# Kernel tuning notes

Measured on AMD Instinct MI355X. Metric: run time of the kernel, lower is better.

## Reference

```python
import jax, jax.numpy as jnp
import numpy as np

NUM_HEADS = 16

def setup_inputs() -> dict:
    key = jax.random.key(0)
    ks = jax.random.split(key, 8)
    T, B, E = 2048, 2, 1024
    s = 1.0 / np.sqrt(E)
    return {
        "query": jax.random.normal(ks[0], (T, B, E), jnp.float32),
        "key": jax.random.normal(ks[1], (T, B, E), jnp.float32),
        "value": jax.random.normal(ks[2], (T, B, E), jnp.float32),
        "Wq": jax.random.normal(ks[3], (E, E), jnp.float32) * s,
        "bq": jnp.zeros((E,), jnp.float32),
        "Wk": jax.random.normal(ks[4], (E, E), jnp.float32) * s,
        "bk": jnp.zeros((E,), jnp.float32),
        "Wv": jax.random.normal(ks[5], (E, E), jnp.float32) * s,
        "bv": jnp.zeros((E,), jnp.float32),
        "Wo": jax.random.normal(ks[6], (E, E), jnp.float32) * s,
        "bo": jnp.zeros((E,), jnp.float32),
    }

def reference(query, key, value, Wq, bq, Wk, bk, Wv, bv, Wo, bo):
    T, B, E = query.shape
    S = key.shape[0]
    H = NUM_HEADS
    hd = E // H
    scaling = float(hd) ** -0.5
    # linear projections (torch Linear: x @ W.T + b)
    q = (query @ Wq.T + bq).reshape(T, B, H, hd)
    k = (key @ Wk.T + bk).reshape(S, B, H, hd)
    v = (value @ Wv.T + bv).reshape(S, B, H, hd)
    # scores: (B, H, T, S)
    scores = jnp.einsum('tbhd,sbhd->bhts', q, k) * scaling
    attn = jax.nn.softmax(scores, axis=-1)  # dropout p=0
    # weighted sum: (T, B, H, hd) -> (T, B, E)
    out = jnp.einsum('bhts,sbhd->tbhd', attn, v).reshape(T, B, E)
    out = out @ Wo.T + bo
    # averaged attention weights over heads: (B, T, S)
    avg_w = attn.mean(axis=1)
    return (out, avg_w)
```

## Files before the change

kernel.cpp:

```cpp
#include <hip/hip_runtime.h>
#include <hip/hip_bf16.h>
#include <stdint.h>

#define HN 16
#define TT 2048
#define BBATCH 2
#define EE 1024
#define HD 64
#define MM 4096

#define SCALEQ 0.18033688011112042f

typedef __attribute__((ext_vector_type(8))) __bf16 bfrag;
typedef __attribute__((ext_vector_type(4))) float f32x4;
typedef __attribute__((ext_vector_type(4))) short s16x4;

__device__ __forceinline__ void gll16(const void* g, void* lds) {
  __builtin_amdgcn_global_load_lds(
      (const __attribute__((address_space(1))) void*)g,
      (__attribute__((address_space(3))) void*)lds, 16, 0, 0);
}

__device__ __forceinline__ f32x4 mfma_bf16(bfrag a, bfrag b, f32x4 c) {
  return __builtin_amdgcn_mfma_f32_16x16x32_bf16(a, b, c, 0, 0, 0);
}

__device__ __forceinline__ const bfrag* fragp(const __bf16* base, int row, int e) {
  return (const bfrag*)(base + row * 64 + ((((e >> 3) ^ row) & 7) << 3));
}
__device__ __forceinline__ void stage8(const __bf16* grow0, int gstride,
                                       __bf16* tile, int r0, int lane) {
  const int rr = lane >> 3;
  const int cl = (lane & 7) ^ rr;
  gll16(grow0 + (size_t)(r0 + rr) * gstride + cl * 8, tile + r0 * 64);
}

__device__ __forceinline__ void barrier_fence() {
  __builtin_amdgcn_s_barrier();
  __builtin_amdgcn_sched_barrier(0);
}

struct CvtArgs {
  const float* src[7];
  __bf16* dst[7];
  int n4[7];
};

__global__ __launch_bounds__(256) void cvt_all(CvtArgs a) {
  const int z = blockIdx.z;
  const int i = blockIdx.x * 256 + threadIdx.x;
  if (i < a.n4[z]) {
    float4 v = ((const float4*)a.src[z])[i];
    struct alignas(8) B4 { __bf16 a0, a1, a2, a3; };
    B4 o = {(__bf16)v.x, (__bf16)v.y, (__bf16)v.z, (__bf16)v.w};
    ((B4*)a.dst[z])[i] = o;
  }
}

template <int MT>
__device__ __forceinline__ void gemm2(const __bf16* __restrict__ X,
                                      const __bf16* __restrict__ W,
                                      const float* __restrict__ bias,
                                      void* __restrict__ out, int mode,
                                      float scale, int m0, int n0,
                                      __bf16* As0, __bf16* As1,
                                      __bf16* Bs0, __bf16* Bs1) {
  const int tid = threadIdx.x, lane = tid & 63, w = tid >> 6;
  const int wm = w >> 1, wn = w & 1;
  const int quad = lane >> 4, l16 = lane & 15;
  constexpr int FM = MT / 32;
  constexpr int NLD = FM + 4;

  auto stageAB = [&](int buf, int k0) {
    __bf16* A = buf ? As1 : As0;
    __bf16* B = buf ? Bs1 : Bs0;
    #pragma unroll
    for (int c = 0; c < FM; ++c)
      stage8(X + (size_t)m0 * EE + k0, EE, A, w * (MT / 4) + c * 8, lane);
    #pragma unroll
    for (int c = 0; c < 4; ++c)
      stage8(W + (size_t)n0 * EE + k0, EE, B, w * 32 + c * 8, lane);
  };

  stageAB(0, 0);

  f32x4 acc[FM][4] = {};

  for (int it = 0; it < EE / 64; ++it) {
    const int cur = it & 1;
    barrier_fence();
    if (it + 1 < EE / 64) {
      stageAB(1 - cur, (it + 1) * 64);
      asm volatile("s_waitcnt vmcnt(%0)" :: "n"(NLD) : "memory");
    } else {
      asm volatile("s_waitcnt vmcnt(0)" ::: "memory");
    }
    barrier_fence();

    const __bf16* A = cur ? As1 : As0;
    const __bf16* B = cur ? Bs1 : Bs0;
    #pragma unroll
    for (int ks = 0; ks < 2; ++ks) {
      bfrag a[FM], b[4];
      #pragma unroll
      for (int f = 0; f < FM; ++f)
        a[f] = *fragp(A, wm * (MT / 2) + f * 16 + l16, ks * 32 + quad * 8);
      #pragma unroll
      for (int f = 0; f < 4; ++f)
        b[f] = *fragp(B, wn * 64 + f * 16 + l16, ks * 32 + quad * 8);
      #pragma unroll
      for (int fm = 0; fm < FM; ++fm)
        #pragma unroll
        for (int fn = 0; fn < 4; ++fn)
          acc[fm][fn] = mfma_bf16(a[fm], b[fn], acc[fm][fn]);
    }
  }

  float bv[4];
  #pragma unroll
  for (int fn = 0; fn < 4; ++fn) bv[fn] = bias[n0 + wn * 64 + fn * 16 + l16];

  #pragma unroll
  for (int fm = 0; fm < FM; ++fm) {
    #pragma unroll
    for (int r = 0; r < 4; ++r) {
      const int gm = m0 + wm * (MT / 2) + fm * 16 + quad * 4 + r;
      #pragma unroll
      for (int fn = 0; fn < 4; ++fn) {
        const int gn = n0 + wn * 64 + fn * 16 + l16;
        const float v = (acc[fm][fn][r] + bv[fn]) * scale;
        if (mode == 0) {
          const int t = gm >> 1, bb = gm & 1, h = gn >> 6, d = gn & 63;
          ((__bf16*)out)[(((size_t)(bb * HN + h)) * TT + t) * HD + d] = (__bf16)v;
        } else if (mode == 2) {
          const int s = gm >> 1, bb = gm & 1, h = gn >> 6, d = gn & 63;
          ((__bf16*)out)[(((size_t)(bb * HN + h)) * HD + d) * TT + s] = (__bf16)v;
        } else {
          ((float*)out)[(size_t)gm * EE + gn] = v;
        }
      }
    }
  }
}

__global__ __launch_bounds__(256, 2) void gemm_qkv(
    const __bf16* __restrict__ xq, const __bf16* __restrict__ xk,
    const __bf16* __restrict__ xv, const __bf16* __restrict__ wq,
    const __bf16* __restrict__ wk, const __bf16* __restrict__ wv,
    const float* __restrict__ bq, const float* __restrict__ bk,
    const float* __restrict__ bv, __bf16* __restrict__ qo,
    __bf16* __restrict__ ko, __bf16* __restrict__ vo) {
  __shared__ __bf16 As[2][128 * 64];
  __shared__ __bf16 Bs[2][128 * 64];
  const int bx = blockIdx.x;
  const int m = bx & 31, n = (bx >> 5) & 7, z = bx >> 8;
  const __bf16 *X, *W;
  const float* bias;
  __bf16* out;
  int mode;
  float scale;
  if (z == 0)      { X = xq; W = wq; bias = bq; out = qo; mode = 0; scale = SCALEQ; }
  else if (z == 1) { X = xk; W = wk; bias = bk; out = ko; mode = 0; scale = 1.0f; }
  else             { X = xv; W = wv; bias = bv; out = vo; mode = 2; scale = 1.0f; }
  gemm2<128>(X, W, bias, out, mode, scale, m * 128, n * 128,
             As[0], As[1], Bs[0], Bs[1]);
}

__global__ __launch_bounds__(256, 2) void attn_fwd(const __bf16* __restrict__ qb,
                                                   const __bf16* __restrict__ kb,
                                                   const __bf16* __restrict__ vtb,
                                                   __bf16* __restrict__ ob,
                                                   float* __restrict__ linv_ws) {
  union Sh {
    __bf16 kv[2][2][2][64 * 64];
    float om[2][64 * 64];
  };
  __shared__ Sh sm;
  __shared__ float Lsum[2][128];
  __shared__ float LinvS[128];

  const int tid = threadIdx.x, lane = tid & 63, w = tid >> 6;
  const int p = w >> 1, tw = w & 1;
  const int quad = lane >> 4, l16 = lane & 15;

  const int bx = blockIdx.x;
  const int xcd = bx & 7, slot = bx >> 3;
  const int bhi = xcd * 4 + (slot >> 4);
  const int t0 = (slot & 15) * 128;
  const int b = bhi >> 4, h = bhi & 15;
  const size_t bh = (size_t)(b * HN + h);

  const __bf16* qbase = qb + (bh * TT + t0) * HD;
  const __bf16* kbase = kb + bh * TT * HD;
  const __bf16* vbase = vtb + bh * HD * TT;
  const int sBase = p * 1024;

  #pragma unroll
  for (int c = 0; c < 4; ++c) {
    stage8(kbase + (size_t)sBase * HD, HD, sm.kv[p][0][0], tw * 32 + c * 8, lane);
    stage8(vbase + sBase, TT, sm.kv[p][1][0], tw * 32 + c * 8, lane);
  }

  bfrag qf[4][2];
  #pragma unroll
  for (int fn = 0; fn < 4; ++fn)
    #pragma unroll
    for (int ks = 0; ks < 2; ++ks)
      qf[fn][ks] = *(const bfrag*)(qbase +
          (size_t)(tw * 64 + fn * 16 + l16) * HD + ks * 32 + quad * 8);

  bfrag ones;
  {
    union { short s[8]; bfrag v; } u;
    #pragma unroll
    for (int i = 0; i < 8; ++i) u.s[i] = 0x3F80;
    ones = u.v;
  }

  f32x4 oacc[4][4] = {};
  f32x4 lacc[4] = {};

  for (int it = 0; it < 16; ++it) {
    const int cur = it & 1;
    barrier_fence();
    if (it + 1 < 16) {
      const int s1 = sBase + (it + 1) * 64;
      #pragma unroll
      for (int c = 0; c < 4; ++c) {
        stage8(kbase + (size_t)s1 * HD, HD, sm.kv[p][0][1 - cur], tw * 32 + c * 8, lane);
        stage8(vbase + s1, TT, sm.kv[p][1][1 - cur], tw * 32 + c * 8, lane);
      }
      asm volatile("s_waitcnt vmcnt(8)" ::: "memory");
    } else {
      asm volatile("s_waitcnt vmcnt(0)" ::: "memory");
    }
    barrier_fence();

    f32x4 sacc[4][4] = {};
    #pragma unroll
    for (int ks = 0; ks < 2; ++ks) {
      bfrag kf[4];
      #pragma unroll
      for (int fm = 0; fm < 4; ++fm)
        kf[fm] = *fragp(sm.kv[p][0][cur], fm * 16 + l16, ks * 32 + quad * 8);
      #pragma unroll
      for (int fm = 0; fm < 4; ++fm)
        #pragma unroll
        for (int fn = 0; fn < 4; ++fn)
          sacc[fm][fn] = mfma_bf16(kf[fm], qf[fn][ks], sacc[fm][fn]);
    }

    union PB { __bf16 hh[8]; bfrag v; } pb[2][4];
    #pragma unroll
    for (int fm = 0; fm < 4; ++fm)
      #pragma unroll
      for (int fn = 0; fn < 4; ++fn) {
        const float p0 = __builtin_amdgcn_exp2f(sacc[fm][fn][0]);
        const float p1 = __builtin_amdgcn_exp2f(sacc[fm][fn][1]);
        const float p2 = __builtin_amdgcn_exp2f(sacc[fm][fn][2]);
        const float p3 = __builtin_amdgcn_exp2f(sacc[fm][fn][3]);
        const int hb = (fm & 1) * 4;
        pb[fm >> 1][fn].hh[hb + 0] = (__bf16)p0;
        pb[fm >> 1][fn].hh[hb + 1] = (__bf16)p1;
        pb[fm >> 1][fn].hh[hb + 2] = (__bf16)p2;
        pb[fm >> 1][fn].hh[hb + 3] = (__bf16)p3;
      }

    #pragma unroll
    for (int ks = 0; ks < 2; ++ks) {
      bfrag vf[4];
      #pragma unroll
      for (int fm = 0; fm < 4; ++fm) {
        const __bf16* base = sm.kv[p][1][cur] + (fm * 16 + l16) * 64;
        const int sw = l16 & 7, qh = quad >> 1, qo = (quad & 1) * 4;
        union VF { s16x4 q[2]; bfrag v; } u;
        u.q[0] = *(const s16x4*)(base + (((ks * 4 + qh) ^ sw) << 3) + qo);
        u.q[1] = *(const s16x4*)(base + (((ks * 4 + 2 + qh) ^ sw) << 3) + qo);
        vf[fm] = u.v;
      }
      #pragma unroll
      for (int fn = 0; fn < 4; ++fn)
        lacc[fn] = mfma_bf16(ones, pb[ks][fn].v, lacc[fn]);
      #pragma unroll
      for (int fm = 0; fm < 4; ++fm)
        #pragma unroll
        for (int fn = 0; fn < 4; ++fn)
          oacc[fm][fn] = mfma_bf16(vf[fm], pb[ks][fn].v, oacc[fm][fn]);
    }
  }

  if (quad == 0)
    #pragma unroll
    for (int fn = 0; fn < 4; ++fn)
      Lsum[p][tw * 64 + fn * 16 + l16] = lacc[fn][0];

  __syncthreads();

  if (p == 1) {
    #pragma unroll
    for (int fm = 0; fm < 4; ++fm)
      #pragma unroll
      for (int fn = 0; fn < 4; ++fn)
        #pragma unroll
        for (int r = 0; r < 4; ++r)
          sm.om[tw][(fm * 16 + quad * 4 + r) * 64 + fn * 16 + l16] = oacc[fm][fn][r];
  }
  if (tid < 128) {
    const float linv = 1.0f / (Lsum[0][tid] + Lsum[1][tid]);
    LinvS[tid] = linv;
    linv_ws[bh * TT + t0 + tid] = linv;
  }
  __syncthreads();

  if (p == 0) {
    float li[4];
    #pragma unroll
    for (int fn = 0; fn < 4; ++fn) li[fn] = LinvS[tw * 64 + fn * 16 + l16];
    #pragma unroll
    for (int fm = 0; fm < 4; ++fm)
      #pragma unroll
      for (int fn = 0; fn < 4; ++fn) {
        const int t = t0 + tw * 64 + fn * 16 + l16;
        struct alignas(8) B4 { __bf16 a0, a1, a2, a3; };
        B4 o;
        __bf16* op = &o.a0;
        #pragma unroll
        for (int r = 0; r < 4; ++r) {
          const float v = (oacc[fm][fn][r] +
              sm.om[tw][(fm * 16 + quad * 4 + r) * 64 + fn * 16 + l16]) * li[fn];
          op[r] = (__bf16)v;
        }
        *(B4*)(ob + ((size_t)t * BBATCH + b) * EE + h * HD + fm * 16 + quad * 4) = o;
      }
  }
}

__device__ __forceinline__ void avg_body(const __bf16* __restrict__ qb,
                                         const __bf16* __restrict__ kb,
                                         const float* __restrict__ linv_ws,
                                         float* __restrict__ avg_out, int bx,
                                         __bf16* Qs0, __bf16* Qs1,
                                         __bf16* Ks0, __bf16* Ks1) {
  const int tid = threadIdx.x, lane = tid & 63, w = tid >> 6;
  const int wm = w >> 1, wn = w & 1;
  const int quad = lane >> 4, l16 = lane & 15;

  const int xcd = bx & 7, slot = bx >> 3;
  const int bti = xcd * 4 + (slot >> 4);
  const int s0 = (slot & 15) * 128;
  const int b = bti >> 4, t0 = (bti & 15) * 128;

  const __bf16* qt = qb + (((size_t)b * HN) * TT + t0) * HD;
  const __bf16* kt = kb + (((size_t)b * HN) * TT + s0) * HD;
  const float* lrow0 = linv_ws + ((size_t)b * HN) * TT + t0 + wm * 64;

  #pragma unroll
  for (int c = 0; c < 4; ++c) {
    stage8(qt, HD, Qs0, w * 32 + c * 8, lane);
    stage8(kt, HD, Ks0, w * 32 + c * 8, lane);
  }

  f32x4 aacc[4][4] = {};

  for (int h = 0; h < HN; ++h) {
    const int cur = h & 1;
    barrier_fence();
    if (h + 1 < HN) {
      const __bf16* qn = qt + (size_t)(h + 1) * TT * HD;
      const __bf16* kn = kt + (size_t)(h + 1) * TT * HD;
      __bf16* Qn = cur ? Qs0 : Qs1;
      __bf16* Kn = cur ? Ks0 : Ks1;
      #pragma unroll
      for (int c = 0; c < 4; ++c) {
        stage8(qn, HD, Qn, w * 32 + c * 8, lane);
        stage8(kn, HD, Kn, w * 32 + c * 8, lane);
      }
      asm volatile("s_waitcnt vmcnt(8)" ::: "memory");
    } else {
      asm volatile("s_waitcnt vmcnt(0)" ::: "memory");
    }
    barrier_fence();

    const __bf16* Qc = cur ? Qs1 : Qs0;
    const __bf16* Kc = cur ? Ks1 : Ks0;
    f32x4 sacc[4][4] = {};
    #pragma unroll
    for (int ks = 0; ks < 2; ++ks) {
      bfrag qf4[4], kf4[4];
      #pragma unroll
      for (int f = 0; f < 4; ++f)
        qf4[f] = *fragp(Qc, wm * 64 + f * 16 + l16, ks * 32 + quad * 8);
      #pragma unroll
      for (int f = 0; f < 4; ++f)
        kf4[f] = *fragp(Kc, wn * 64 + f * 16 + l16, ks * 32 + quad * 8);
      #pragma unroll
      for (int fm = 0; fm < 4; ++fm)
        #pragma unroll
        for (int fn = 0; fn < 4; ++fn)
          sacc[fm][fn] = mfma_bf16(qf4[fm], kf4[fn], sacc[fm][fn]);
    }

    const float* lr = lrow0 + (size_t)h * TT;
    f32x4 lvv[4];
    #pragma unroll
    for (int fm = 0; fm < 4; ++fm)
      lvv[fm] = *(const f32x4*)(lr + fm * 16 + quad * 4);

    #pragma unroll
    for (int fm = 0; fm < 4; ++fm)
      #pragma unroll
      for (int fn = 0; fn < 4; ++fn)
        #pragma unroll
        for (int r = 0; r < 4; ++r)
          aacc[fm][fn][r] += __builtin_amdgcn_exp2f(sacc[fm][fn][r]) * lvv[fm][r];
  }

  const float invh = 1.0f / (float)HN;
  #pragma unroll
  for (int fm = 0; fm < 4; ++fm)
    #pragma unroll
    for (int r = 0; r < 4; ++r) {
      const int t = t0 + wm * 64 + fm * 16 + quad * 4 + r;
      #pragma unroll
      for (int fn = 0; fn < 4; ++fn) {
        const int s = s0 + wn * 64 + fn * 16 + l16;
        avg_out[((size_t)b * TT + t) * TT + s] = aacc[fm][fn][r] * invh;
      }
    }
}

struct TailAvg { __bf16 Qs[2][128 * 64]; __bf16 Ks[2][128 * 64]; };
struct TailGo  { __bf16 As[2][64 * 64];  __bf16 Bs[2][128 * 64]; };
union TailSh { TailAvg a; TailGo g; };

__global__ __launch_bounds__(256, 2) void tail_fused(
    const __bf16* __restrict__ qb, const __bf16* __restrict__ kb,
    const float* __restrict__ linv_ws, float* __restrict__ avg_out,
    const __bf16* __restrict__ ob, const __bf16* __restrict__ wo,
    const float* __restrict__ bo, float* __restrict__ out) {
  __shared__ TailSh sh;
  const int bx = blockIdx.x;
  if (bx < 512) {
    avg_body(qb, kb, linv_ws, avg_out, bx,
             sh.a.Qs[0], sh.a.Qs[1], sh.a.Ks[0], sh.a.Ks[1]);
  } else {
    const int b2 = bx - 512;
    const int m = b2 & 63, n = b2 >> 6;
    gemm2<64>(ob, wo, bo, out, 3, 1.0f, m * 64, n * 128,
              sh.g.As[0], sh.g.As[1], sh.g.Bs[0], sh.g.Bs[1]);
  }
}

extern "C" void kernel_launch(void* const* d_in, const int* in_sizes, int n_in,
                              void* d_out, int out_size, void* d_ws, size_t ws_size,
                              hipStream_t stream) {
  (void)in_sizes; (void)n_in; (void)out_size; (void)ws_size;
  const float* query = (const float*)d_in[0];
  const float* key   = (const float*)d_in[1];
  const float* value = (const float*)d_in[2];
  const float* Wq = (const float*)d_in[3];
  const float* bq = (const float*)d_in[4];
  const float* Wk = (const float*)d_in[5];
  const float* bk = (const float*)d_in[6];
  const float* Wv = (const float*)d_in[7];
  const float* bv = (const float*)d_in[8];
  const float* Wo = (const float*)d_in[9];
  const float* bo = (const float*)d_in[10];

  char* ws = (char*)d_ws;
  size_t off = 0;
  auto wsalloc = [&](size_t bytes) -> void* {
    void* p = ws + off;
    off += (bytes + 255) & ~(size_t)255;
    return p;
  };
  const size_t XE = (size_t)MM * EE;
  const size_t WE = (size_t)EE * EE;
  __bf16* xq   = (__bf16*)wsalloc(XE * 2);
  __bf16* xk   = (__bf16*)wsalloc(XE * 2);
  __bf16* xv   = (__bf16*)wsalloc(XE * 2);
  __bf16* wqb  = (__bf16*)wsalloc(WE * 2);
  __bf16* wkb  = (__bf16*)wsalloc(WE * 2);
  __bf16* wvb  = (__bf16*)wsalloc(WE * 2);
  __bf16* wob  = (__bf16*)wsalloc(WE * 2);
  __bf16* qbuf = (__bf16*)wsalloc(XE * 2);
  __bf16* kbuf = (__bf16*)wsalloc(XE * 2);
  __bf16* vtbuf= (__bf16*)wsalloc(XE * 2);
  __bf16* obuf = (__bf16*)wsalloc(XE * 2);
  float* linv  = (float*)wsalloc((size_t)BBATCH * HN * TT * 4);

  CvtArgs ca;
  ca.src[0] = query; ca.dst[0] = xq;  ca.n4[0] = (int)(XE / 4);
  ca.src[1] = key;   ca.dst[1] = xk;  ca.n4[1] = (int)(XE / 4);
  ca.src[2] = value; ca.dst[2] = xv;  ca.n4[2] = (int)(XE / 4);
  ca.src[3] = Wq;    ca.dst[3] = wqb; ca.n4[3] = (int)(WE / 4);
  ca.src[4] = Wk;    ca.dst[4] = wkb; ca.n4[4] = (int)(WE / 4);
  ca.src[5] = Wv;    ca.dst[5] = wvb; ca.n4[5] = (int)(WE / 4);
  ca.src[6] = Wo;    ca.dst[6] = wob; ca.n4[6] = (int)(WE / 4);
  cvt_all<<<dim3(4096, 1, 7), 256, 0, stream>>>(ca);

  gemm_qkv<<<dim3(768), 256, 0, stream>>>(xq, xk, xv, wqb, wkb, wvb,
                                          bq, bk, bv, qbuf, kbuf, vtbuf);

  attn_fwd<<<dim3(512), 256, 0, stream>>>(qbuf, kbuf, vtbuf, obuf, linv);

  float* avg_out = (float*)d_out + (size_t)TT * BBATCH * EE;
  tail_fused<<<dim3(1024), 256, 0, stream>>>(qbuf, kbuf, linv, avg_out,
                                             obuf, wob, bo, (float*)d_out);
}
```

Baseline: 240.5 us.

## Fuse kernels into two persistent launches joined by grid barriers

Folds the fp32-to-bf16 conversion into the QKV GEMM kernel, and the attention kernel into the tail kernel. Each pair is separated by a software grid barrier built on an atomic counter, which cuts four launches to two and removes the inter-kernel gaps. The QKV GEMM drops double buffering for a single LDS buffer at higher occupancy. The shared GEMM helper replaces its explicit vmcnt pipelining with plain __syncthreads. The grid barriers assume every block is resident at once and can deadlock otherwise. The extra synchronisation and the loss of load/compute overlap may cost more than the launches saved.

Result: slower. 483.3 us (+100.9%).

```diff
diff --git a/kernel.cpp b/kernel.cpp
--- a/kernel.cpp
+++ b/kernel.cpp
@@ -15,6 +15,8 @@
 typedef __attribute__((ext_vector_type(4))) float f32x4;
 typedef __attribute__((ext_vector_type(4))) short s16x4;
 
+struct alignas(8) B4 { __bf16 a0, a1, a2, a3; };
+
 __device__ __forceinline__ void gll16(const void* g, void* lds) {
   __builtin_amdgcn_global_load_lds(
       (const __attribute__((address_space(1))) void*)g,
@@ -40,21 +42,19 @@
   __builtin_amdgcn_sched_barrier(0);
 }
 
-struct CvtArgs {
-  const float* src[7];
-  __bf16* dst[7];
-  int n4[7];
-};
-
-__global__ __launch_bounds__(256) void cvt_all(CvtArgs a) {
-  const int z = blockIdx.z;
-  const int i = blockIdx.x * 256 + threadIdx.x;
-  if (i < a.n4[z]) {
-    float4 v = ((const float4*)a.src[z])[i];
-    struct alignas(8) B4 { __bf16 a0, a1, a2, a3; };
-    B4 o = {(__bf16)v.x, (__bf16)v.y, (__bf16)v.z, (__bf16)v.w};
-    ((B4*)a.dst[z])[i] = o;
-  }
+__device__ __forceinline__ void grid_barrier(unsigned int* ctr, unsigned int nb) {
+  __syncthreads();
+  if (threadIdx.x == 0) {
+    __threadfence();
+    unsigned int old = __hip_atomic_fetch_add(ctr, 1u, __ATOMIC_RELEASE,
+                                              __HIP_MEMORY_SCOPE_AGENT);
+    unsigned int target = old - (old % nb) + nb;
+    while (__hip_atomic_load(ctr, __ATOMIC_ACQUIRE,
+                             __HIP_MEMORY_SCOPE_AGENT) < target)
+      __builtin_amdgcn_s_sleep(2);
+    __threadfence();
+  }
+  __syncthreads();
 }
 
 template <int MT>
@@ -69,7 +69,6 @@
   const int wm = w >> 1, wn = w & 1;
   const int quad = lane >> 4, l16 = lane & 15;
   constexpr int FM = MT / 32;
-  constexpr int NLD = FM + 4;
 
   auto stageAB = [&](int buf, int k0) {
     __bf16* A = buf ? As1 : As0;
@@ -88,14 +87,8 @@
 
   for (int it = 0; it < EE / 64; ++it) {
     const int cur = it & 1;
-    barrier_fence();
-    if (it + 1 < EE / 64) {
-      stageAB(1 - cur, (it + 1) * 64);
-      asm volatile("s_waitcnt vmcnt(%0)" :: "n"(NLD) : "memory");
-    } else {
-      asm volatile("s_waitcnt vmcnt(0)" ::: "memory");
-    }
-    barrier_fence();
+    __syncthreads();
+    if (it + 1 < EE / 64) stageAB(1 - cur, (it + 1) * 64);
 
     const __bf16* A = cur ? As1 : As0;
     const __bf16* B = cur ? Bs1 : Bs0;
@@ -143,15 +136,39 @@
   }
 }
 
-__global__ __launch_bounds__(256, 2) void gemm_qkv(
-    const __bf16* __restrict__ xq, const __bf16* __restrict__ xk,
-    const __bf16* __restrict__ xv, const __bf16* __restrict__ wq,
-    const __bf16* __restrict__ wk, const __bf16* __restrict__ wv,
-    const float* __restrict__ bq, const float* __restrict__ bk,
-    const float* __restrict__ bv, __bf16* __restrict__ qo,
-    __bf16* __restrict__ ko, __bf16* __restrict__ vo) {
-  __shared__ __bf16 As[2][128 * 64];
-  __shared__ __bf16 Bs[2][128 * 64];
+struct Fused1 {
+  const float* src[7];
+  __bf16* dst[7];
+  const float* bias[3];
+  __bf16* outp[3];
+  unsigned int* ctr;
+};
+
+__global__ __launch_bounds__(256, 4) void cvt_gemm_qkv(Fused1 a) {
+  __shared__ __bf16 As[128 * 64];
+  __shared__ __bf16 Bs[128 * 64];
+
+  {
+    const int gtid = blockIdx.x * 256 + threadIdx.x;
+    const int gstr = 768 * 256;
+    for (int z = 0; z < 7; ++z) {
+      const int n4 = (z < 3) ? (1 << 20) : (1 << 18);
+      const float4* s = (const float4*)a.src[z];
+      B4* d = (B4*)a.dst[z];
+      for (int i = gtid; i < n4; i += gstr) {
+        float4 v = s[i];
+        B4 o = {(__bf16)v.x, (__bf16)v.y, (__bf16)v.z, (__bf16)v.w};
+        d[i] = o;
+      }
+    }
+  }
+
+  grid_barrier(a.ctr, 768);
+
+  const int tid = threadIdx.x, lane = tid & 63, w = tid >> 6;
+  const int wm = w >> 1, wn = w & 1;
+  const int quad = lane >> 4, l16 = lane & 15;
+
   const int bx = blockIdx.x;
   const int m = bx & 31, n = (bx >> 5) & 7, z = bx >> 8;
   const __bf16 *X, *W;
@@ -159,31 +176,80 @@
   __bf16* out;
   int mode;
   float scale;
-  if (z == 0)      { X = xq; W = wq; bias = bq; out = qo; mode = 0; scale = SCALEQ; }
-  else if (z == 1) { X = xk; W = wk; bias = bk; out = ko; mode = 0; scale = 1.0f; }
-  else             { X = xv; W = wv; bias = bv; out = vo; mode = 2; scale = 1.0f; }
-  gemm2<128>(X, W, bias, out, mode, scale, m * 128, n * 128,
-             As[0], As[1], Bs[0], Bs[1]);
-}
-
-__global__ __launch_bounds__(256, 2) void attn_fwd(const __bf16* __restrict__ qb,
-                                                   const __bf16* __restrict__ kb,
-                                                   const __bf16* __restrict__ vtb,
-                                                   __bf16* __restrict__ ob,
-                                                   float* __restrict__ linv_ws) {
-  union Sh {
-    __bf16 kv[2][2][2][64 * 64];
-    float om[2][64 * 64];
-  };
-  __shared__ Sh sm;
-  __shared__ float Lsum[2][128];
-  __shared__ float LinvS[128];
-
+  if (z == 0)      { X = a.dst[0]; W = a.dst[3]; bias = a.bias[0]; out = a.outp[0]; mode = 0; scale = SCALEQ; }
+  else if (z == 1) { X = a.dst[1]; W = a.dst[4]; bias = a.bias[1]; out = a.outp[1]; mode = 0; scale = 1.0f; }
+  else             { X = a.dst[2]; W = a.dst[5]; bias = a.bias[2]; out = a.outp[2]; mode = 2; scale = 1.0f; }
+  const int m0 = m * 128, n0 = n * 128;
+
+  f32x4 acc[4][4] = {};
+
+  for (int it = 0; it < 16; ++it) {
+    const int k0 = it * 64;
+    #pragma unroll
+    for (int c = 0; c < 4; ++c)
+      stage8(X + (size_t)m0 * EE + k0, EE, As, w * 32 + c * 8, lane);
+    #pragma unroll
+    for (int c = 0; c < 4; ++c)
+      stage8(W + (size_t)n0 * EE + k0, EE, Bs, w * 32 + c * 8, lane);
+    __syncthreads();
+    #pragma unroll
+    for (int ks = 0; ks < 2; ++ks) {
+      bfrag af[4], bf[4];
+      #pragma unroll
+      for (int f = 0; f < 4; ++f)
+        af[f] = *fragp(As, wm * 64 + f * 16 + l16, ks * 32 + quad * 8);
+      #pragma unroll
+      for (int f = 0; f < 4; ++f)
+        bf[f] = *fragp(Bs, wn * 64 + f * 16 + l16, ks * 32 + quad * 8);
+      #pragma unroll
+      for (int fm = 0; fm < 4; ++fm)
+        #pragma unroll
+        for (int fn = 0; fn < 4; ++fn)
+          acc[fm][fn] = mfma_bf16(af[fm], bf[fn], acc[fm][fn]);
+    }
+    __syncthreads();
+  }
+
+  float bvv[4];
+  #pragma unroll
+  for (int fn = 0; fn < 4; ++fn) bvv[fn] = bias[n0 + wn * 64 + fn * 16 + l16];
+
+  #pragma unroll
+  for (int fm = 0; fm < 4; ++fm) {
+    #pragma unroll
+    for (int r = 0; r < 4; ++r) {
+      const int gm = m0 + wm * 64 + fm * 16 + quad * 4 + r;
+      #pragma unroll
+      for (int fn = 0; fn < 4; ++fn) {
+        const int gn = n0 + wn * 64 + fn * 16 + l16;
+        const float v = (acc[fm][fn][r] + bvv[fn]) * scale;
+        if (mode == 0) {
+          const int t = gm >> 1, bb = gm & 1, h = gn >> 6, d = gn & 63;
+          out[(((size_t)(bb * HN + h)) * TT + t) * HD + d] = (__bf16)v;
+        } else {
+          const int s = gm >> 1, bb = gm & 1, h = gn >> 6, d = gn & 63;
+          out[(((size_t)(bb * HN + h)) * HD + d) * TT + s] = (__bf16)v;
+        }
+      }
+    }
+  }
+}
+
+struct AttnSh {
+  union { __bf16 kv[2][2][2][64 * 64]; float om[2][64 * 64]; } u;
+  float Lsum[2][128];
+  float LinvS[128];
+};
+
+__device__ void attn_body(const __bf16* __restrict__ qb,
+                          const __bf16* __restrict__ kb,
+                          const __bf16* __restrict__ vtb,
+                          __bf16* __restrict__ ob,
+                          float* __restrict__ linv_ws, int bx, AttnSh& sa) {
   const int tid = threadIdx.x, lane = tid & 63, w = tid >> 6;
   const int p = w >> 1, tw = w & 1;
   const int quad = lane >> 4, l16 = lane & 15;
 
-  const int bx = blockIdx.x;
   const int xcd = bx & 7, slot = bx >> 3;
   const int bhi = xcd * 4 + (slot >> 4);
   const int t0 = (slot & 15) * 128;
@@ -197,8 +263,8 @@
 
   #pragma unroll
   for (int c = 0; c < 4; ++c) {
-    stage8(kbase + (size_t)sBase * HD, HD, sm.kv[p][0][0], tw * 32 + c * 8, lane);
-    stage8(vbase + sBase, TT, sm.kv[p][1][0], tw * 32 + c * 8, lane);
+    stage8(kbase + (size_t)sBase * HD, HD, sa.u.kv[p][0][0], tw * 32 + c * 8, lane);
+    stage8(vbase + sBase, TT, sa.u.kv[p][1][0], tw * 32 + c * 8, lane);
   }
 
   bfrag qf[4][2];
@@ -227,8 +293,8 @@
       const int s1 = sBase + (it + 1) * 64;
       #pragma unroll
       for (int c = 0; c < 4; ++c) {
-        stage8(kbase + (size_t)s1 * HD, HD, sm.kv[p][0][1 - cur], tw * 32 + c * 8, lane);
-        stage8(vbase + s1, TT, sm.kv[p][1][1 - cur], tw * 32 + c * 8, lane);
+        stage8(kbase + (size_t)s1 * HD, HD, sa.u.kv[p][0][1 - cur], tw * 32 + c * 8, lane);
+        stage8(vbase + s1, TT, sa.u.kv[p][1][1 - cur], tw * 32 + c * 8, lane);
       }
       asm volatile("s_waitcnt vmcnt(8)" ::: "memory");
     } else {
@@ -242,7 +308,7 @@
       bfrag kf[4];
       #pragma unroll
       for (int fm = 0; fm < 4; ++fm)
-        kf[fm] = *fragp(sm.kv[p][0][cur], fm * 16 + l16, ks * 32 + quad * 8);
+        kf[fm] = *fragp(sa.u.kv[p][0][cur], fm * 16 + l16, ks * 32 + quad * 8);
       #pragma unroll
       for (int fm = 0; fm < 4; ++fm)
         #pragma unroll
@@ -271,7 +337,7 @@
       bfrag vf[4];
       #pragma unroll
       for (int fm = 0; fm < 4; ++fm) {
-        const __bf16* base = sm.kv[p][1][cur] + (fm * 16 + l16) * 64;
+        const __bf16* base = sa.u.kv[p][1][cur] + (fm * 16 + l16) * 64;
         const int sw = l16 & 7, qh = quad >> 1, qo = (quad & 1) * 4;
         union VF { s16x4 q[2]; bfrag v; } u;
         u.q[0] = *(const s16x4*)(base + (((ks * 4 + qh) ^ sw) << 3) + qo);
@@ -292,7 +358,7 @@
   if (quad == 0)
     #pragma unroll
     for (int fn = 0; fn < 4; ++fn)
-      Lsum[p][tw * 64 + fn * 16 + l16] = lacc[fn][0];
+      sa.Lsum[p][tw * 64 + fn * 16 + l16] = lacc[fn][0];
 
   __syncthreads();
 
@@ -303,11 +369,11 @@
       for (int fn = 0; fn < 4; ++fn)
         #pragma unroll
         for (int r = 0; r < 4; ++r)
-          sm.om[tw][(fm * 16 + quad * 4 + r) * 64 + fn * 16 + l16] = oacc[fm][fn][r];
+          sa.u.om[tw][(fm * 16 + quad * 4 + r) * 64 + fn * 16 + l16] = oacc[fm][fn][r];
   }
   if (tid < 128) {
-    const float linv = 1.0f / (Lsum[0][tid] + Lsum[1][tid]);
-    LinvS[tid] = linv;
+    const float linv = 1.0f / (sa.Lsum[0][tid] + sa.Lsum[1][tid]);
+    sa.LinvS[tid] = linv;
     linv_ws[bh * TT + t0 + tid] = linv;
   }
   __syncthreads();
@@ -315,19 +381,18 @@
   if (p == 0) {
     float li[4];
     #pragma unroll
-    for (int fn = 0; fn < 4; ++fn) li[fn] = LinvS[tw * 64 + fn * 16 + l16];
+    for (int fn = 0; fn < 4; ++fn) li[fn] = sa.LinvS[tw * 64 + fn * 16 + l16];
     #pragma unroll
     for (int fm = 0; fm < 4; ++fm)
       #pragma unroll
       for (int fn = 0; fn < 4; ++fn) {
         const int t = t0 + tw * 64 + fn * 16 + l16;
-        struct alignas(8) B4 { __bf16 a0, a1, a2, a3; };
         B4 o;
         __bf16* op = &o.a0;
         #pragma unroll
         for (int r = 0; r < 4; ++r) {
           const float v = (oacc[fm][fn][r] +
-              sm.om[tw][(fm * 16 + quad * 4 + r) * 64 + fn * 16 + l16]) * li[fn];
+              sa.u.om[tw][(fm * 16 + quad * 4 + r) * 64 + fn * 16 + l16]) * li[fn];
           op[r] = (__bf16)v;
         }
         *(B4*)(ob + ((size_t)t * BBATCH + b) * EE + h * HD + fm * 16 + quad * 4) = o;
@@ -335,12 +400,12 @@
   }
 }
 
-__device__ __forceinline__ void avg_body(const __bf16* __restrict__ qb,
-                                         const __bf16* __restrict__ kb,
-                                         const float* __restrict__ linv_ws,
-                                         float* __restrict__ avg_out, int bx,
-                                         __bf16* Qs0, __bf16* Qs1,
-                                         __bf16* Ks0, __bf16* Ks1) {
+__device__ void avg_body(const __bf16* __restrict__ qb,
+                         const __bf16* __restrict__ kb,
+                         const float* __restrict__ linv_ws,
+                         float* __restrict__ avg_out, int bx,
+                         __bf16* Qs0, __bf16* Qs1,
+                         __bf16* Ks0, __bf16* Ks1) {
   const int tid = threadIdx.x, lane = tid & 63, w = tid >> 6;
   const int wm = w >> 1, wn = w & 1;
   const int quad = lane >> 4, l16 = lane & 15;
@@ -431,22 +496,33 @@
 
 struct TailAvg { __bf16 Qs[2][128 * 64]; __bf16 Ks[2][128 * 64]; };
 struct TailGo  { __bf16 As[2][64 * 64];  __bf16 Bs[2][128 * 64]; };
-union TailSh { TailAvg a; TailGo g; };
-
-__global__ __launch_bounds__(256, 2) void tail_fused(
+union Sh2 { AttnSh at; TailAvg a; TailGo g; };
+
+__global__ __launch_bounds__(256, 2) void attn_tail(
     const __bf16* __restrict__ qb, const __bf16* __restrict__ kb,
-    const float* __restrict__ linv_ws, float* __restrict__ avg_out,
-    const __bf16* __restrict__ ob, const __bf16* __restrict__ wo,
-    const float* __restrict__ bo, float* __restrict__ out) {
-  __shared__ TailSh sh;
+    const __bf16* __restrict__ vtb, __bf16* __restrict__ ob,
+    float* __restrict__ linv_ws, float* __restrict__ avg_out,
+    const __bf16* __restrict__ wo, const float* __restrict__ bo,
+    float* __restrict__ out, unsigned int* ctr) {
+  __shared__ Sh2 sh;
   const int bx = blockIdx.x;
-  if (bx < 512) {
+
+  attn_body(qb, kb, vtb, ob, linv_ws, bx, sh.at);
+
+  grid_barrier(ctr, 512);
+
+  const int gm_m = bx & 63, gm_n = bx >> 6;
+  if ((bx >> 8) & 1) {
+    gemm2<64>(ob, wo, bo, out, 3, 1.0f, gm_m * 64, gm_n * 128,
+              sh.g.As[0], sh.g.As[1], sh.g.Bs[0], sh.g.Bs[1]);
+    __syncthreads();
     avg_body(qb, kb, linv_ws, avg_out, bx,
              sh.a.Qs[0], sh.a.Qs[1], sh.a.Ks[0], sh.a.Ks[1]);
   } else {
-    const int b2 = bx - 512;
-    const int m = b2 & 63, n = b2 >> 6;
-    gemm2<64>(ob, wo, bo, out, 3, 1.0f, m * 64, n * 128,
+    avg_body(qb, kb, linv_ws, avg_out, bx,
+             sh.a.Qs[0], sh.a.Qs[1], sh.a.Ks[0], sh.a.Ks[1]);
+    __syncthreads();
+    gemm2<64>(ob, wo, bo, out, 3, 1.0f, gm_m * 64, gm_n * 128,
               sh.g.As[0], sh.g.As[1], sh.g.Bs[0], sh.g.Bs[1]);
   }
 }
@@ -488,23 +564,23 @@
   __bf16* vtbuf= (__bf16*)wsalloc(XE * 2);
   __bf16* obuf = (__bf16*)wsalloc(XE * 2);
   float* linv  = (float*)wsalloc((size_t)BBATCH * HN * TT * 4);
-
-  CvtArgs ca;
-  ca.src[0] = query; ca.dst[0] = xq;  ca.n4[0] = (int)(XE / 4);
-  ca.src[1] = key;   ca.dst[1] = xk;  ca.n4[1] = (int)(XE / 4);
-  ca.src[2] = value; ca.dst[2] = xv;  ca.n4[2] = (int)(XE / 4);
-  ca.src[3] = Wq;    ca.dst[3] = wqb; ca.n4[3] = (int)(WE / 4);
-  ca.src[4] = Wk;    ca.dst[4] = wkb; ca.n4[4] = (int)(WE / 4);
-  ca.src[5] = Wv;    ca.dst[5] = wvb; ca.n4[5] = (int)(WE / 4);
-  ca.src[6] = Wo;    ca.dst[6] = wob; ca.n4[6] = (int)(WE / 4);
-  cvt_all<<<dim3(4096, 1, 7), 256, 0, stream>>>(ca);
-
-  gemm_qkv<<<dim3(768), 256, 0, stream>>>(xq, xk, xv, wqb, wkb, wvb,
-                                          bq, bk, bv, qbuf, kbuf, vtbuf);
-
-  attn_fwd<<<dim3(512), 256, 0, stream>>>(qbuf, kbuf, vtbuf, obuf, linv);
+  unsigned int* ctrs = (unsigned int*)wsalloc(512);
+
+  hipMemsetAsync(ctrs, 0, 512, stream);
+
+  Fused1 f1;
+  f1.src[0] = query; f1.src[1] = key; f1.src[2] = value;
+  f1.src[3] = Wq;    f1.src[4] = Wk;  f1.src[5] = Wv;  f1.src[6] = Wo;
+  f1.dst[0] = xq;    f1.dst[1] = xk;  f1.dst[2] = xv;
+  f1.dst[3] = wqb;   f1.dst[4] = wkb; f1.dst[5] = wvb; f1.dst[6] = wob;
+  f1.bias[0] = bq;   f1.bias[1] = bk; f1.bias[2] = bv;
+  f1.outp[0] = qbuf; f1.outp[1] = kbuf; f1.outp[2] = vtbuf;
+  f1.ctr = ctrs;
+
+  cvt_gemm_qkv<<<dim3(768), 256, 0, stream>>>(f1);
 
   float* avg_out = (float*)d_out + (size_t)TT * BBATCH * EE;
-  tail_fused<<<dim3(1024), 256, 0, stream>>>(qbuf, kbuf, linv, avg_out,
-                                             obuf, wob, bo, (float*)d_out);
-}
+  attn_tail<<<dim3(512), 256, 0, stream>>>(qbuf, kbuf, vtbuf, obuf, linv,
+                                           avg_out, wob, bo, (float*)d_out,
+                                           ctrs + 64);
+}
```

## Fuse fp32-to-bf16 conversion into GEMM tile loads and drop separate convert kernel

Applied to the files above, without the earlier changes.

Removes the standalone cvt_all kernel that converted inputs and weights to bf16. The QKV GEMM and the output-projection GEMM now read fp32 directly from global memory into registers, convert to bf16, and write swizzled tiles to LDS, using a register-prefetch double-buffer pipeline in place of async global_load_lds. This saves one kernel launch and a full read+write pass over about 60 MB of inputs. In exchange the GEMMs read twice as many bytes per tile, hold more registers, and do the conversion on the critical path, which could lower occupancy or MFMA utilisation.

After: 267.8 us. 1.11x slower.

```diff
diff --git a/kernel.cpp b/kernel.cpp
--- a/kernel.cpp
+++ b/kernel.cpp
@@ -15,6 +15,9 @@
 typedef __attribute__((ext_vector_type(4))) float f32x4;
 typedef __attribute__((ext_vector_type(4))) short s16x4;
 
+struct alignas(8) B4 { __bf16 a0, a1, a2, a3; };
+struct alignas(16) B8 { __bf16 h[8]; };
+
 __device__ __forceinline__ void gll16(const void* g, void* lds) {
   __builtin_amdgcn_global_load_lds(
       (const __attribute__((address_space(1))) void*)g,
@@ -40,130 +43,223 @@
   __builtin_amdgcn_sched_barrier(0);
 }
 
-struct CvtArgs {
-  const float* src[7];
-  __bf16* dst[7];
-  int n4[7];
-};
-
-__global__ __launch_bounds__(256) void cvt_all(CvtArgs a) {
-  const int z = blockIdx.z;
-  const int i = blockIdx.x * 256 + threadIdx.x;
-  if (i < a.n4[z]) {
-    float4 v = ((const float4*)a.src[z])[i];
-    struct alignas(8) B4 { __bf16 a0, a1, a2, a3; };
-    B4 o = {(__bf16)v.x, (__bf16)v.y, (__bf16)v.z, (__bf16)v.w};
-    ((B4*)a.dst[z])[i] = o;
-  }
-}
-
-template <int MT>
-__device__ __forceinline__ void gemm2(const __bf16* __restrict__ X,
-                                      const __bf16* __restrict__ W,
-                                      const float* __restrict__ bias,
-                                      void* __restrict__ out, int mode,
-                                      float scale, int m0, int n0,
-                                      __bf16* As0, __bf16* As1,
-                                      __bf16* Bs0, __bf16* Bs1) {
-  const int tid = threadIdx.x, lane = tid & 63, w = tid >> 6;
-  const int wm = w >> 1, wn = w & 1;
-  const int quad = lane >> 4, l16 = lane & 15;
-  constexpr int FM = MT / 32;
-  constexpr int NLD = FM + 4;
-
-  auto stageAB = [&](int buf, int k0) {
-    __bf16* A = buf ? As1 : As0;
-    __bf16* B = buf ? Bs1 : Bs0;
-    #pragma unroll
-    for (int c = 0; c < FM; ++c)
-      stage8(X + (size_t)m0 * EE + k0, EE, A, w * (MT / 4) + c * 8, lane);
-    #pragma unroll
-    for (int c = 0; c < 4; ++c)
-      stage8(W + (size_t)n0 * EE + k0, EE, B, w * 32 + c * 8, lane);
-  };
-
-  stageAB(0, 0);
-
-  f32x4 acc[FM][4] = {};
-
-  for (int it = 0; it < EE / 64; ++it) {
-    const int cur = it & 1;
-    barrier_fence();
-    if (it + 1 < EE / 64) {
-      stageAB(1 - cur, (it + 1) * 64);
-      asm volatile("s_waitcnt vmcnt(%0)" :: "n"(NLD) : "memory");
-    } else {
-      asm volatile("s_waitcnt vmcnt(0)" ::: "memory");
-    }
-    barrier_fence();
-
-    const __bf16* A = cur ? As1 : As0;
-    const __bf16* B = cur ? Bs1 : Bs0;
-    #pragma unroll
-    for (int ks = 0; ks < 2; ++ks) {
-      bfrag a[FM], b[4];
-      #pragma unroll
-      for (int f = 0; f < FM; ++f)
-        a[f] = *fragp(A, wm * (MT / 2) + f * 16 + l16, ks * 32 + quad * 8);
-      #pragma unroll
-      for (int f = 0; f < 4; ++f)
-        b[f] = *fragp(B, wn * 64 + f * 16 + l16, ks * 32 + quad * 8);
-      #pragma unroll
-      for (int fm = 0; fm < FM; ++fm)
-        #pragma unroll
-        for (int fn = 0; fn < 4; ++fn)
-          acc[fm][fn] = mfma_bf16(a[fm], b[fn], acc[fm][fn]);
-    }
-  }
-
-  float bv[4];
-  #pragma unroll
-  for (int fn = 0; fn < 4; ++fn) bv[fn] = bias[n0 + wn * 64 + fn * 16 + l16];
-
-  #pragma unroll
-  for (int fm = 0; fm < FM; ++fm) {
-    #pragma unroll
-    for (int r = 0; r < 4; ++r) {
-      const int gm = m0 + wm * (MT / 2) + fm * 16 + quad * 4 + r;
-      #pragma unroll
-      for (int fn = 0; fn < 4; ++fn) {
-        const int gn = n0 + wn * 64 + fn * 16 + l16;
-        const float v = (acc[fm][fn][r] + bv[fn]) * scale;
-        if (mode == 0) {
-          const int t = gm >> 1, bb = gm & 1, h = gn >> 6, d = gn & 63;
-          ((__bf16*)out)[(((size_t)(bb * HN + h)) * TT + t) * HD + d] = (__bf16)v;
-        } else if (mode == 2) {
-          const int s = gm >> 1, bb = gm & 1, h = gn >> 6, d = gn & 63;
-          ((__bf16*)out)[(((size_t)(bb * HN + h)) * HD + d) * TT + s] = (__bf16)v;
-        } else {
-          ((float*)out)[(size_t)gm * EE + gn] = v;
-        }
-      }
-    }
-  }
+__device__ __forceinline__ void lbar() {
+  __builtin_amdgcn_sched_barrier(0);
+  asm volatile("s_waitcnt lgkmcnt(0)" ::: "memory");
+  __builtin_amdgcn_s_barrier();
+  __builtin_amdgcn_sched_barrier(0);
 }
 
 __global__ __launch_bounds__(256, 2) void gemm_qkv(
-    const __bf16* __restrict__ xq, const __bf16* __restrict__ xk,
-    const __bf16* __restrict__ xv, const __bf16* __restrict__ wq,
-    const __bf16* __restrict__ wk, const __bf16* __restrict__ wv,
+    const float* __restrict__ xq, const float* __restrict__ xk,
+    const float* __restrict__ xv, const float* __restrict__ wq,
+    const float* __restrict__ wk, const float* __restrict__ wv,
     const float* __restrict__ bq, const float* __restrict__ bk,
     const float* __restrict__ bv, __bf16* __restrict__ qo,
     __bf16* __restrict__ ko, __bf16* __restrict__ vo) {
   __shared__ __bf16 As[2][128 * 64];
   __shared__ __bf16 Bs[2][128 * 64];
+  const int tid = threadIdx.x, lane = tid & 63, w = tid >> 6;
+  const int wm = w >> 1, wn = w & 1;
+  const int quad = lane >> 4, l16 = lane & 15;
+
   const int bx = blockIdx.x;
   const int m = bx & 31, n = (bx >> 5) & 7, z = bx >> 8;
-  const __bf16 *X, *W;
-  const float* bias;
+  const float *X, *W, *bias;
   __bf16* out;
   int mode;
   float scale;
   if (z == 0)      { X = xq; W = wq; bias = bq; out = qo; mode = 0; scale = SCALEQ; }
   else if (z == 1) { X = xk; W = wk; bias = bk; out = ko; mode = 0; scale = 1.0f; }
   else             { X = xv; W = wv; bias = bv; out = vo; mode = 2; scale = 1.0f; }
-  gemm2<128>(X, W, bias, out, mode, scale, m * 128, n * 128,
-             As[0], As[1], Bs[0], Bs[1]);
+  const int m0 = m * 128, n0 = n * 128;
+  const float* Xg = X + (size_t)m0 * EE;
+  const float* Wg = W + (size_t)n0 * EE;
+
+  const int rA = tid >> 3;
+  const int cc = tid & 7;
+
+  float4 vA[8], vB[8];
+
+  auto loadT = [&](const float* src, int k0, float4* dst) {
+    #pragma unroll
+    for (int i = 0; i < 4; ++i) {
+      const float* p = src + (size_t)(rA + 32 * i) * EE + k0 + cc * 8;
+      dst[2 * i]     = *(const float4*)p;
+      dst[2 * i + 1] = *(const float4*)(p + 4);
+    }
+  };
+  auto writeT = [&](__bf16* tile, const float4* v) {
+    #pragma unroll
+    for (int i = 0; i < 4; ++i) {
+      const int r = rA + 32 * i;
+      B8 o;
+      o.h[0] = (__bf16)v[2 * i].x;     o.h[1] = (__bf16)v[2 * i].y;
+      o.h[2] = (__bf16)v[2 * i].z;     o.h[3] = (__bf16)v[2 * i].w;
+      o.h[4] = (__bf16)v[2 * i + 1].x; o.h[5] = (__bf16)v[2 * i + 1].y;
+      o.h[6] = (__bf16)v[2 * i + 1].z; o.h[7] = (__bf16)v[2 * i + 1].w;
+      *(B8*)(tile + r * 64 + (((cc ^ r) & 7) << 3)) = o;
+    }
+  };
+
+  loadT(Xg, 0, vA);  loadT(Wg, 0, vB);
+  writeT(As[0], vA); writeT(Bs[0], vB);
+  loadT(Xg, 64, vA); loadT(Wg, 64, vB);
+
+  f32x4 acc[4][4] = {};
+
+  for (int it = 0; it < 16; ++it) {
+    const int cur = it & 1;
+    lbar();
+
+    const __bf16* A = As[cur];
+    const __bf16* B = Bs[cur];
+    #pragma unroll
+    for (int ks = 0; ks < 2; ++ks) {
+      bfrag af[4], bf[4];
+      #pragma unroll
+      for (int f = 0; f < 4; ++f)
+        af[f] = *fragp(A, wm * 64 + f * 16 + l16, ks * 32 + quad * 8);
+      #pragma unroll
+      for (int f = 0; f < 4; ++f)
+        bf[f] = *fragp(B, wn * 64 + f * 16 + l16, ks * 32 + quad * 8);
+      #pragma unroll
+      for (int fm = 0; fm < 4; ++fm)
+        #pragma unroll
+        for (int fn = 0; fn < 4; ++fn)
+          acc[fm][fn] = mfma_bf16(af[fm], bf[fn], acc[fm][fn]);
+    }
+
+    if (it + 1 < 16) {
+      writeT(As[1 - cur], vA);
+      writeT(Bs[1 - cur], vB);
+    }
+    if (it + 2 < 16) {
+      loadT(Xg, (it + 2) * 64, vA);
+      loadT(Wg, (it + 2) * 64, vB);
+    }
+  }
+
+  float bvv[4];
+  #pragma unroll
+  for (int fn = 0; fn < 4; ++fn) bvv[fn] = bias[n0 + wn * 64 + fn * 16 + l16];
+
+  #pragma unroll
+  for (int fm = 0; fm < 4; ++fm) {
+    #pragma unroll
+    for (int r = 0; r < 4; ++r) {
+      const int gm = m0 + wm * 64 + fm * 16 + quad * 4 + r;
+      #pragma unroll
+      for (int fn = 0; fn < 4; ++fn) {
+        const int gn = n0 + wn * 64 + fn * 16 + l16;
+        const float v = (acc[fm][fn][r] + bvv[fn]) * scale;
+        if (mode == 0) {
+          const int t = gm >> 1, bb = gm & 1, h = gn >> 6, d = gn & 63;
+          out[(((size_t)(bb * HN + h)) * TT + t) * HD + d] = (__bf16)v;
+        } else {
+          const int s = gm >> 1, bb = gm & 1, h = gn >> 6, d = gn & 63;
+          out[(((size_t)(bb * HN + h)) * HD + d) * TT + s] = (__bf16)v;
+        }
+      }
+    }
+  }
+}
+
+__device__ __forceinline__ void gemm2o(const __bf16* __restrict__ X,
+                                       const float* __restrict__ W,
+                                       const float* __restrict__ bias,
+                                       float* __restrict__ out,
+                                       int m0, int n0,
+                                       __bf16* As0, __bf16* As1,
+                                       __bf16* Bs0, __bf16* Bs1) {
+  const int tid = threadIdx.x, lane = tid & 63, w = tid >> 6;
+  const int wm = w >> 1, wn = w & 1;
+  const int quad = lane >> 4, l16 = lane & 15;
+  const int rA = tid >> 3, cc = tid & 7;
+  const float* Wg = W + (size_t)n0 * EE;
+
+  float4 vB[8];
+  auto loadB = [&](int k0) {
+    #pragma unroll
+    for (int i = 0; i < 4; ++i) {
+      const float* p = Wg + (size_t)(rA + 32 * i) * EE + k0 + cc * 8;
+      vB[2 * i]     = *(const float4*)p;
+      vB[2 * i + 1] = *(const float4*)(p + 4);
+    }
+  };
+  auto writeB = [&](__bf16* tile) {
+    #pragma unroll
+    for (int i = 0; i < 4; ++i) {
+      const int r = rA + 32 * i;
+      B8 o;
+      o.h[0] = (__bf16)vB[2 * i].x;     o.h[1] = (__bf16)vB[2 * i].y;
+      o.h[2] = (__bf16)vB[2 * i].z;     o.h[3] = (__bf16)vB[2 * i].w;
+      o.h[4] = (__bf16)vB[2 * i + 1].x; o.h[5] = (__bf16)vB[2 * i + 1].y;
+      o.h[6] = (__bf16)vB[2 * i + 1].z; o.h[7] = (__bf16)vB[2 * i + 1].w;
+      *(B8*)(tile + r * 64 + (((cc ^ r) & 7) << 3)) = o;
+    }
+  };
+  auto stageA = [&](__bf16* A, int k0) {
+    #pragma unroll
+    for (int c = 0; c < 2; ++c)
+      stage8(X + (size_t)m0 * EE + k0, EE, A, w * 16 + c * 8, lane);
+  };
+
+  stageA(As0, 0);
+  loadB(0);
+  writeB(Bs0);
+  loadB(64);
+
+  f32x4 acc[2][4] = {};
+
+  for (int it = 0; it < 16; ++it) {
+    const int cur = it & 1;
+    __builtin_amdgcn_sched_barrier(0);
+    if (it == 15) asm volatile("s_waitcnt vmcnt(0) lgkmcnt(0)" ::: "memory");
+    else          asm volatile("s_waitcnt vmcnt(8) lgkmcnt(0)" ::: "memory");
+    __builtin_amdgcn_s_barrier();
+    __builtin_amdgcn_sched_barrier(0);
+
+    if (it + 1 < 16) stageA(cur ? As0 : As1, (it + 1) * 64);
+
+    const __bf16* A = cur ? As1 : As0;
+    const __bf16* B = cur ? Bs1 : Bs0;
+    #pragma unroll
+    for (int ks = 0; ks < 2; ++ks) {
+      bfrag af[2], bf[4];
+      #pragma unroll
+      for (int f = 0; f < 2; ++f)
+        af[f] = *fragp(A, wm * 32 + f * 16 + l16, ks * 32 + quad * 8);
+      #pragma unroll
+      for (int f = 0; f < 4; ++f)
+        bf[f] = *fragp(B, wn * 64 + f * 16 + l16, ks * 32 + quad * 8);
+      #pragma unroll
+      for (int fm = 0; fm < 2; ++fm)
+        #pragma unroll
+        for (int fn = 0; fn < 4; ++fn)
+          acc[fm][fn] = mfma_bf16(af[fm], bf[fn], acc[fm][fn]);
+    }
+
+    if (it + 1 < 16) writeB(cur ? Bs0 : Bs1);
+    if (it + 2 < 16) loadB((it + 2) * 64);
+  }
+
+  float bvv[4];
+  #pragma unroll
+  for (int fn = 0; fn < 4; ++fn) bvv[fn] = bias[n0 + wn * 64 + fn * 16 + l16];
+
+  #pragma unroll
+  for (int fm = 0; fm < 2; ++fm) {
+    #pragma unroll
+    for (int r = 0; r < 4; ++r) {
+      const int gm = m0 + wm * 32 + fm * 16 + quad * 4 + r;
+      #pragma unroll
+      for (int fn = 0; fn < 4; ++fn) {
+        const int gn = n0 + wn * 64 + fn * 16 + l16;
+        out[(size_t)gm * EE + gn] = acc[fm][fn][r] + bvv[fn];
+      }
+    }
+  }
 }
 
 __global__ __launch_bounds__(256, 2) void attn_fwd(const __bf16* __restrict__ qb,
@@ -321,7 +417,6 @@
       #pragma unroll
       for (int fn = 0; fn < 4; ++fn) {
         const int t = t0 + tw * 64 + fn * 16 + l16;
-        struct alignas(8) B4 { __bf16 a0, a1, a2, a3; };
         B4 o;
         __bf16* op = &o.a0;
         #pragma unroll
@@ -335,12 +430,12 @@
   }
 }
 
-__device__ __forceinline__ void avg_body(const __bf16* __restrict__ qb,
-                                         const __bf16* __restrict__ kb,
-                                         const float* __restrict__ linv_ws,
-                                         float* __restrict__ avg_out, int bx,
-                                         __bf16* Qs0, __bf16* Qs1,
-                                         __bf16* Ks0, __bf16* Ks1) {
+__device__ void avg_body(const __bf16* __restrict__ qb,
+                         const __bf16* __restrict__ kb,
+                         const float* __restrict__ linv_ws,
+                         float* __restrict__ avg_out, int bx,
+                         __bf16* Qs0, __bf16* Qs1,
+                         __bf16* Ks0, __bf16* Ks1) {
   const int tid = threadIdx.x, lane = tid & 63, w = tid >> 6;
   const int wm = w >> 1, wn = w & 1;
   const int quad = lane >> 4, l16 = lane & 15;
@@ -436,7 +531,7 @@
 __global__ __launch_bounds__(256, 2) void tail_fused(
     const __bf16* __restrict__ qb, const __bf16* __restrict__ kb,
     const float* __restrict__ linv_ws, float* __restrict__ avg_out,
-    const __bf16* __restrict__ ob, const __bf16* __restrict__ wo,
+    const __bf16* __restrict__ ob, const float* __restrict__ wo,
     const float* __restrict__ bo, float* __restrict__ out) {
   __shared__ TailSh sh;
   const int bx = blockIdx.x;
@@ -446,8 +541,8 @@
   } else {
     const int b2 = bx - 512;
     const int m = b2 & 63, n = b2 >> 6;
-    gemm2<64>(ob, wo, bo, out, 3, 1.0f, m * 64, n * 128,
-              sh.g.As[0], sh.g.As[1], sh.g.Bs[0], sh.g.Bs[1]);
+    gemm2o(ob, wo, bo, out, m * 64, n * 128,
+           sh.g.As[0], sh.g.As[1], sh.g.Bs[0], sh.g.Bs[1]);
   }
 }
 
@@ -475,36 +570,18 @@
     return p;
   };
   const size_t XE = (size_t)MM * EE;
-  const size_t WE = (size_t)EE * EE;
-  __bf16* xq   = (__bf16*)wsalloc(XE * 2);
-  __bf16* xk   = (__bf16*)wsalloc(XE * 2);
-  __bf16* xv   = (__bf16*)wsalloc(XE * 2);
-  __bf16* wqb  = (__bf16*)wsalloc(WE * 2);
-  __bf16* wkb  = (__bf16*)wsalloc(WE * 2);
-  __bf16* wvb  = (__bf16*)wsalloc(WE * 2);
-  __bf16* wob  = (__bf16*)wsalloc(WE * 2);
   __bf16* qbuf = (__bf16*)wsalloc(XE * 2);
   __bf16* kbuf = (__bf16*)wsalloc(XE * 2);
   __bf16* vtbuf= (__bf16*)wsalloc(XE * 2);
   __bf16* obuf = (__bf16*)wsalloc(XE * 2);
   float* linv  = (float*)wsalloc((size_t)BBATCH * HN * TT * 4);
 
-  CvtArgs ca;
-  ca.src[0] = query; ca.dst[0] = xq;  ca.n4[0] = (int)(XE / 4);
-  ca.src[1] = key;   ca.dst[1] = xk;  ca.n4[1] = (int)(XE / 4);
-  ca.src[2] = value; ca.dst[2] = xv;  ca.n4[2] = (int)(XE / 4);
-  ca.src[3] = Wq;    ca.dst[3] = wqb; ca.n4[3] = (int)(WE / 4);
-  ca.src[4] = Wk;    ca.dst[4] = wkb; ca.n4[4] = (int)(WE / 4);
-  ca.src[5] = Wv;    ca.dst[5] = wvb; ca.n4[5] = (int)(WE / 4);
-  ca.src[6] = Wo;    ca.dst[6] = wob; ca.n4[6] = (int)(WE / 4);
-  cvt_all<<<dim3(4096, 1, 7), 256, 0, stream>>>(ca);
-
-  gemm_qkv<<<dim3(768), 256, 0, stream>>>(xq, xk, xv, wqb, wkb, wvb,
+  gemm_qkv<<<dim3(768), 256, 0, stream>>>(query, key, value, Wq, Wk, Wv,
                                           bq, bk, bv, qbuf, kbuf, vtbuf);
 
   attn_fwd<<<dim3(512), 256, 0, stream>>>(qbuf, kbuf, vtbuf, obuf, linv);
 
   float* avg_out = (float*)d_out + (size_t)TT * BBATCH * EE;
   tail_fused<<<dim3(1024), 256, 0, stream>>>(qbuf, kbuf, linv, avg_out,
-                                             obuf, wob, bo, (float*)d_out);
-}
+                                             obuf, Wo, bo, (float*)d_out);
+}
```
